# Performance work log

Measured on AMD Instinct MI355X. Metric: run time of the kernel, lower is better.

The kernel has to match this reference:

```python
import jax, jax.numpy as jnp
import numpy as np

D = 512      # d_model
H = 8        # num_heads
DH = D // H  # d_head = 64
WIN = 10     # window_size
DFF = 2048   # d_ff
EPS = 1e-5   # LayerNorm eps


def _layernorm(x, w, b):
    mu = jnp.mean(x, axis=-1, keepdims=True)
    var = jnp.mean(jnp.square(x - mu), axis=-1, keepdims=True)
    return (x - mu) * jax.lax.rsqrt(var + EPS) * w + b


def setup_inputs() -> dict:
    key = jax.random.key(0)
    ks = jax.random.split(key, 8)
    s = 0.02
    inp = {
        "z": jax.random.normal(ks[0], (4, 2048, D), jnp.float32),
        "Wq": jax.random.normal(ks[1], (D, D), jnp.float32) * s,
        "bq": jnp.zeros((D,), jnp.float32),
        "Wk": jax.random.normal(ks[2], (D, D), jnp.float32) * s,
        "bk": jnp.zeros((D,), jnp.float32),
        "Wv": jax.random.normal(ks[3], (D, D), jnp.float32) * s,
        "bv": jnp.zeros((D,), jnp.float32),
        "Wo": jax.random.normal(ks[4], (D, D), jnp.float32) * s,
        "bo": jnp.zeros((D,), jnp.float32),
        "ln1_w": jnp.ones((D,), jnp.float32),
        "ln1_b": jnp.zeros((D,), jnp.float32),
        "W1": jax.random.normal(ks[5], (D, DFF), jnp.float32) * s,
        "b1": jnp.zeros((DFF,), jnp.float32),
        "W2": jax.random.normal(ks[6], (DFF, D), jnp.float32) * s,
        "b2": jnp.zeros((D,), jnp.float32),
        "ln2_w": jnp.ones((D,), jnp.float32),
        "ln2_b": jnp.zeros((D,), jnp.float32),
    }
    return inp


def reference(z, Wq, bq, Wk, bk, Wv, bv, Wo, bo, ln1_w, ln1_b, W1, b1, W2, b2, ln2_w, ln2_b):
    B, T, Dm = z.shape
    # projections -> [B, H, T, DH]
    q = (z @ Wq + bq).reshape(B, T, H, DH).transpose(0, 2, 1, 3)
    k = (z @ Wk + bk).reshape(B, T, H, DH).transpose(0, 2, 1, 3)
    v = (z @ Wv + bv).reshape(B, T, H, DH).transpose(0, 2, 1, 3)
    scale = 1.0 / jnp.sqrt(jnp.asarray(DH, z.dtype))
    scores = jnp.einsum('bhqd,bhkd->bhqk', q, k) * scale  # [B,H,T,T]
    idx = jnp.arange(T)
    dist = idx[:, None] - idx[None, :]
    valid = (dist >= 0) & (dist < WIN)
    neg = jnp.finfo(scores.dtype).min
    scores = jnp.where(valid[None, None], scores, neg)
    attn = jax.nn.softmax(scores, axis=-1)  # dropout is identity in eval
    out = jnp.einsum('bhqk,bhkd->bhqd', attn, v)
    out = out.transpose(0, 2, 1, 3).reshape(B, T, Dm)
    out = out @ Wo + bo
    z = _layernorm(z + out, ln1_w, ln1_b)
    # FFN with exact (erf) GELU, matching torch nn.GELU default
    ff = jax.nn.gelu(z @ W1 + b1, approximate=False) @ W2 + b2
    z = _layernorm(z + ff, ln2_w, ln2_b)
    return z
```

## Files before the change

### kernel.cpp

```cpp
#include <hip/hip_runtime.h>
#include <cstdint>
#include <cstddef>

#define DEV __device__ __forceinline__

typedef __bf16 bf16x8 __attribute__((ext_vector_type(8)));
typedef float f32x4 __attribute__((ext_vector_type(4)));
typedef unsigned short us8 __attribute__((ext_vector_type(8)));
typedef unsigned short us4 __attribute__((ext_vector_type(4)));

typedef const __attribute__((address_space(1))) unsigned int GUI;
typedef __attribute__((address_space(3))) unsigned int LUI;

DEV unsigned short f2bf(float f) {
  unsigned int u = __builtin_bit_cast(unsigned int, f);
  u += 0x7fffu + ((u >> 16) & 1u);
  return (unsigned short)(u >> 16);
}
DEV float bf2f(unsigned short h) {
  unsigned int u = ((unsigned int)h) << 16;
  return __builtin_bit_cast(float, u);
}

DEV float gelu_exact(float x) {
  float xs = x * 0.70710678118654752f;
  float a = fabsf(xs);
  float t = __builtin_amdgcn_rcpf(fmaf(0.3275911f, a, 1.0f));
  float poly = t * fmaf(t, fmaf(t, fmaf(t, fmaf(t, 1.061405429f, -1.453152027f),
                                        1.421413741f), -0.284496736f), 0.254829592f);
  float erfa = 1.0f - poly * __expf(-a * a);
  float er = (xs < 0.f) ? -erfa : erfa;
  return 0.5f * x * (1.0f + er);
}

DEV void tr32(const float* __restrict__ in, unsigned short* __restrict__ out,
              int K, int N, int k0, int n0) {
  __shared__ float tile[32][33];
  const int tx = threadIdx.x & 31, ty = threadIdx.x >> 5;
#pragma unroll
  for (int i = 0; i < 32; i += 8)
    tile[ty + i][tx] = in[(size_t)(k0 + ty + i) * N + n0 + tx];
  __syncthreads();
#pragma unroll
  for (int i = 0; i < 32; i += 8)
    out[(size_t)(n0 + ty + i) * K + k0 + tx] = f2bf(tile[tx][ty + i]);
}

__global__ __launch_bounds__(256) void k_prep(
    const float* __restrict__ z, unsigned short* __restrict__ zb,
    const float* __restrict__ Wq, const float* __restrict__ Wk,
    const float* __restrict__ Wv, const float* __restrict__ Wo,
    unsigned short* __restrict__ Wsq,
    const float* __restrict__ W1, unsigned short* __restrict__ W1T,
    const float* __restrict__ W2, unsigned short* __restrict__ W2T,
    const float* __restrict__ bq, const float* __restrict__ bk,
    const float* __restrict__ bv, float* __restrict__ biasqkv) {
  const int j = blockIdx.x;
  const int tid = threadIdx.x;
  if (j < 4096) {
    int i = j * 256 + tid;
    float4 v = ((const float4*)z)[i];
    us4 o;
    o.x = f2bf(v.x); o.y = f2bf(v.y); o.z = f2bf(v.z); o.w = f2bf(v.w);
    *(us4*)(zb + (size_t)i * 4) = o;
  } else if (j < 5120) {
    int t = j - 4096;
    int mat = t >> 8, tile = t & 255;
    const float* in = mat == 0 ? Wq : mat == 1 ? Wk : mat == 2 ? Wv : Wo;
    tr32(in, Wsq + (size_t)mat * 262144, 512, 512, (tile >> 4) * 32, (tile & 15) * 32);
  } else if (j < 6144) {
    int t = j - 5120;
    tr32(W1, W1T, 512, 2048, (t / 64) * 32, (t % 64) * 32);
  } else if (j < 7168) {
    int t = j - 6144;
    tr32(W2, W2T, 2048, 512, (t / 16) * 32, (t % 16) * 32);
  } else {
    for (int i = tid; i < 1536; i += 256)
      biasqkv[i] = (i < 512) ? bq[i] : (i < 1024 ? bk[i - 512] : bv[i - 1024]);
  }
}

template <int MODE, int SPLITK>
DEV void gemm256_body(const unsigned short* __restrict__ A,
                      const unsigned short* __restrict__ BT,
                      const float* __restrict__ bias,
                      unsigned short* __restrict__ outp,
                      int K, int N) {
  __shared__ __align__(16) unsigned short As[2 * 16384];
  __shared__ __align__(16) unsigned short Bs[2 * 16384];
  const int tid = threadIdx.x;
  const int wave = tid >> 6, lane = tid & 63;
  const int wm = wave >> 2, wn = wave & 3;

  const int nx = gridDim.x, ny = gridDim.y;
  const int nwg = nx * ny * SPLITK;
  const int lid = (blockIdx.z * ny + blockIdx.y) * nx + blockIdx.x;
  const int q8 = nwg >> 3, r8 = nwg & 7;
  const int xcd = lid & 7, slot = lid >> 3;
  const int wid = (xcd < r8 ? xcd * (q8 + 1) : r8 * (q8 + 1) + (xcd - r8) * q8) + slot;
  const int nbz = nx * SPLITK;
  const int bxz = wid % nbz;
  const int by  = wid / nbz;
  const int bx  = bxz % nx;
  const int z   = bxz / nx;

  const int rbase = by * 256;
  const int nbase = bx * 256;
  const int nkt = (K / SPLITK) >> 6;
  const int kb = z * (K / SPLITK);

  float bv_[4];
#pragma unroll
  for (int n = 0; n < 4; ++n) {
    int gcol = nbase + wn * 64 + n * 16 + (lane & 15);
    bv_[n] = (z == 0) ? bias[gcol] : 0.f;
  }
  asm volatile("s_waitcnt vmcnt(0)" ::: "memory");

  auto STAGE = [&](int buf, int k0) {
#pragma unroll
    for (int t = 0; t < 4; ++t) {
      int s = t * 512 + tid;
      int row = s >> 3;
      int col = ((s & 7) ^ (row & 7)) << 3;
      const unsigned short* ga = A + (size_t)(rbase + row) * K + k0 + col;
      const unsigned short* gb = BT + (size_t)(nbase + row) * K + k0 + col;
      const int dst = buf * 16384 + (t * 512 + wave * 64) * 8;
      __builtin_amdgcn_global_load_lds((GUI*)ga, (LUI*)(As + dst), 16, 0, 0);
      __builtin_amdgcn_global_load_lds((GUI*)gb, (LUI*)(Bs + dst), 16, 0, 0);
    }
  };

  f32x4 acc[8][4] = {};
  STAGE(0, kb);

  for (int kt = 0; kt < nkt; ++kt) {
    const int cur = kt & 1;
    if (kt + 1 < nkt) {
      STAGE(cur ^ 1, kb + (kt + 1) * 64);
      asm volatile("s_waitcnt vmcnt(8)" ::: "memory");
    } else {
      asm volatile("s_waitcnt vmcnt(0)" ::: "memory");
    }
    __builtin_amdgcn_s_barrier();

#pragma unroll
    for (int ks = 0; ks < 2; ++ks) {
      bf16x8 af[8], bfr[4];
#pragma unroll
      for (int m = 0; m < 8; ++m) {
        int row = wm * 128 + m * 16 + (lane & 15);
        int ch = (ks * 4 + (lane >> 4)) ^ (row & 7);
        af[m] = __builtin_bit_cast(bf16x8, *(const us8*)(As + cur * 16384 + row * 64 + ch * 8));
      }
#pragma unroll
      for (int n = 0; n < 4; ++n) {
        int row = wn * 64 + n * 16 + (lane & 15);
        int ch = (ks * 4 + (lane >> 4)) ^ (row & 7);
        bfr[n] = __builtin_bit_cast(bf16x8, *(const us8*)(Bs + cur * 16384 + row * 64 + ch * 8));
      }
      __builtin_amdgcn_s_setprio(1);
#pragma unroll
      for (int m = 0; m < 8; ++m)
#pragma unroll
        for (int n = 0; n < 4; ++n)
          acc[m][n] = __builtin_amdgcn_mfma_f32_16x16x32_bf16(af[m], bfr[n], acc[m][n], 0, 0, 0);
      __builtin_amdgcn_s_setprio(0);
    }
    asm volatile("s_waitcnt lgkmcnt(0)" ::: "memory");
    __builtin_amdgcn_s_barrier();
  }

  unsigned short* opv = outp + (size_t)z * 8192 * N;
#pragma unroll
  for (int m = 0; m < 8; ++m) {
    int grow0 = rbase + wm * 128 + m * 16 + ((lane >> 4) << 2);
#pragma unroll
    for (int n = 0; n < 4; ++n) {
      int gcol = nbase + wn * 64 + n * 16 + (lane & 15);
#pragma unroll
      for (int r = 0; r < 4; ++r) {
        float v = acc[m][n][r] + bv_[n];
        if (MODE == 2) v = gelu_exact(v);
        opv[(size_t)(grow0 + r) * N + gcol] = f2bf(v);
      }
    }
  }
}

__global__ __launch_bounds__(512) void k_qkv(const unsigned short* __restrict__ A,
                                             const unsigned short* __restrict__ BT,
                                             const float* __restrict__ bias,
                                             unsigned short* __restrict__ outp, int K, int N) {
  gemm256_body<0, 1>(A, BT, bias, outp, K, N);
}
__global__ __launch_bounds__(512) void k_ffn1(const unsigned short* __restrict__ A,
                                              const unsigned short* __restrict__ BT,
                                              const float* __restrict__ bias,
                                              unsigned short* __restrict__ outp, int K, int N) {
  gemm256_body<2, 1>(A, BT, bias, outp, K, N);
}
__global__ __launch_bounds__(512) void k_ffn2(const unsigned short* __restrict__ A,
                                              const unsigned short* __restrict__ BT,
                                              const float* __restrict__ bias,
                                              unsigned short* __restrict__ outp, int K, int N) {
  gemm256_body<0, 4>(A, BT, bias, outp, K, N);
}

__global__ __launch_bounds__(512) void k_awl(
    const unsigned short* __restrict__ qkv,
    const unsigned short* __restrict__ WoT,
    const float* __restrict__ bo,
    const unsigned short* __restrict__ zb,
    const float* __restrict__ ln1w, const float* __restrict__ ln1b,
    unsigned short* __restrict__ z1b) {
  __shared__ __align__(16) char smem[137728];
  unsigned short* aout = (unsigned short*)smem;
  float* Kt = (float*)(smem + 33280);
  float* P  = (float*)(smem + 125440);
  unsigned short* Bst = (unsigned short*)(smem + 33280);
  float* part = (float*)(smem + 98816);
  float* lnp  = (float*)(smem + 100864);

  const int tid = threadIdx.x;
  const int w = tid >> 6, lane = tid & 63;
  const int bid = blockIdx.x;
  const int b = bid >> 6;
  const int i0 = (bid & 63) * 32;
  const int b2048 = b * 2048;
  const int h64 = w * 64;

  float* KtH = Kt + w * (64 * 45);
#pragma unroll 8
  for (int r = 0; r < 41; ++r) {
    int jloc = i0 - 9 + r;
    int jc = jloc < 0 ? 0 : jloc;
    KtH[lane * 45 + r] = bf2f(qkv[(size_t)(b2048 + jc) * 1536 + 512 + h64 + lane]);
  }
  const int qe = lane & 31, dh = lane >> 5;
  us8 qreg[4];
  {
    const unsigned short* qp = qkv + (size_t)(b2048 + i0 + qe) * 1536 + h64 + dh * 32;
#pragma unroll
    for (int t = 0; t < 4; ++t) qreg[t] = *(const us8*)(qp + t * 8);
  }
  float s[10];
#pragma unroll
  for (int jj = 0; jj < 10; ++jj) s[jj] = 0.f;
#pragma unroll
  for (int t = 0; t < 4; ++t) {
#pragma unroll
    for (int e = 0; e < 8; ++e) {
      float qd = bf2f(qreg[t][e]);
      int d = dh * 32 + t * 8 + e;
#pragma unroll
      for (int jj = 0; jj < 10; ++jj)
        s[jj] = fmaf(qd, KtH[d * 45 + qe + jj], s[jj]);
    }
  }
#pragma unroll
  for (int jj = 0; jj < 10; ++jj) s[jj] += __shfl_xor(s[jj], 32);
  const int iG = i0 + qe;
#pragma unroll
  for (int jj = 0; jj < 10; ++jj)
    s[jj] = (iG - 9 + jj >= 0) ? s[jj] * 0.125f : -1e30f;
  float mx = s[9];
#pragma unroll
  for (int jj = 0; jj < 9; ++jj) mx = fmaxf(mx, s[jj]);
  float den = 0.f;
#pragma unroll
  for (int jj = 0; jj < 10; ++jj) {
    s[jj] = __expf(s[jj] - mx);
    den += s[jj];
  }
  float inv = 1.f / den;
  if (lane < 32) {
#pragma unroll
    for (int jj = 0; jj < 10; ++jj) P[(w * 32 + qe) * 12 + jj] = s[jj] * inv;
  }
  for (int q0 = 0; q0 < 32; q0 += 4) {
    float vv[13];
#pragma unroll
    for (int t = 0; t < 13; ++t) {
      int jloc = i0 + q0 - 9 + t;
      int jc = jloc < 0 ? 0 : jloc;
      vv[t] = bf2f(qkv[(size_t)(b2048 + jc) * 1536 + 1024 + h64 + lane]);
    }
#pragma unroll
    for (int qq = 0; qq < 4; ++qq) {
      const int qy = q0 + qq;
      const float* pp = &P[(w * 32 + qy) * 12];
      float o = 0.f;
#pragma unroll
      for (int jj = 0; jj < 10; ++jj) o = fmaf(pp[jj], vv[qq + jj], o);
      aout[qy * 520 + h64 + lane] = f2bf(o);
    }
  }
  __syncthreads();

  const int q4 = lane >> 4, l15 = lane & 15;
  auto STAGE = [&](int buf, int k0) {
#pragma unroll
    for (int t = 0; t < 4; ++t) {
      int sI = t * 512 + tid;
      int R = sI >> 3;
      int c = (sI & 7) ^ (R & 7);
      int rr = 2 * R + (c >> 2);
      int kl = (c & 3) << 3;
      const unsigned short* gb = WoT + (size_t)rr * 512 + k0 + kl;
      const int dst = buf * 16384 + (t * 512 + w * 64) * 8;
      __builtin_amdgcn_global_load_lds((GUI*)gb, (LUI*)(Bst + dst), 16, 0, 0);
    }
  };
  asm volatile("s_waitcnt vmcnt(0)" ::: "memory");
  STAGE(0, 0);
  f32x4 acc[2][4] = {};
  for (int kt = 0; kt < 16; ++kt) {
    const int cur = kt & 1;
    if (kt + 1 < 16) {
      STAGE(cur ^ 1, (kt + 1) * 32);
      asm volatile("s_waitcnt vmcnt(4)" ::: "memory");
    } else {
      asm volatile("s_waitcnt vmcnt(0)" ::: "memory");
    }
    __builtin_amdgcn_s_barrier();
    bf16x8 af[2], bfr[4];
#pragma unroll
    for (int m = 0; m < 2; ++m) {
      int row = m * 16 + l15;
      af[m] = __builtin_bit_cast(bf16x8, *(const us8*)(aout + row * 520 + kt * 32 + q4 * 8));
    }
#pragma unroll
    for (int n = 0; n < 4; ++n) {
      int rr = h64 + n * 16 + l15;
      int R = rr >> 1;
      int d = (((rr & 1) << 2) + q4) ^ (R & 7);
      bfr[n] = __builtin_bit_cast(bf16x8, *(const us8*)(Bst + cur * 16384 + R * 64 + d * 8));
    }
    asm volatile("s_waitcnt lgkmcnt(0)" ::: "memory");
    __builtin_amdgcn_sched_barrier(0);
    __builtin_amdgcn_s_setprio(1);
#pragma unroll
    for (int m = 0; m < 2; ++m)
#pragma unroll
      for (int n = 0; n < 4; ++n)
        acc[m][n] = __builtin_amdgcn_mfma_f32_16x16x32_bf16(af[m], bfr[n], acc[m][n], 0, 0, 0);
    __builtin_amdgcn_s_setprio(0);
    __builtin_amdgcn_s_barrier();
  }

  float x[2][4][4];
  float psum[8], pss[8];
#pragma unroll
  for (int m = 0; m < 8; ++m) { psum[m] = 0.f; pss[m] = 0.f; }
#pragma unroll
  for (int m = 0; m < 2; ++m) {
#pragma unroll
    for (int n = 0; n < 4; ++n) {
      int col = h64 + n * 16 + l15;
      float bv = bo[col];
#pragma unroll
      for (int r = 0; r < 4; ++r) {
        int row = m * 16 + (q4 << 2) + r;
        float v = acc[m][n][r] + bv + bf2f(zb[(size_t)(b2048 + i0 + row) * 512 + col]);
        x[m][n][r] = v;
        psum[m * 4 + r] += v;
        pss[m * 4 + r] += v * v;
      }
    }
  }
#pragma unroll
  for (int m = 0; m < 8; ++m) {
#pragma unroll
    for (int o = 1; o < 16; o <<= 1) {
      psum[m] += __shfl_xor(psum[m], o);
      pss[m]  += __shfl_xor(pss[m], o);
    }
  }
  if (l15 == 0) {
#pragma unroll
    for (int m = 0; m < 2; ++m)
#pragma unroll
      for (int r = 0; r < 4; ++r) {
        int row = m * 16 + (q4 << 2) + r;
        part[(row * 8 + w) * 2 + 0] = psum[m * 4 + r];
        part[(row * 8 + w) * 2 + 1] = pss[m * 4 + r];
      }
  }
  __syncthreads();
  if (w == 0 && lane < 32) {
    float su = 0.f, ssq = 0.f;
#pragma unroll
    for (int p = 0; p < 8; ++p) {
      su  += part[(lane * 8 + p) * 2 + 0];
      ssq += part[(lane * 8 + p) * 2 + 1];
    }
    float mu = su * (1.f / 512.f);
    float var = ssq * (1.f / 512.f) - mu * mu;
    lnp[lane * 2 + 0] = mu;
    lnp[lane * 2 + 1] = rsqrtf(var + 1e-5f);
  }
  __syncthreads();
#pragma unroll
  for (int m = 0; m < 2; ++m) {
#pragma unroll
    for (int n = 0; n < 4; ++n) {
      int col = h64 + n * 16 + l15;
      float wv = ln1w[col], bbv = ln1b[col];
#pragma unroll
      for (int r = 0; r < 4; ++r) {
        int row = m * 16 + (q4 << 2) + r;
        float o = (x[m][n][r] - lnp[row * 2]) * lnp[row * 2 + 1] * wv + bbv;
        z1b[(size_t)(b2048 + i0 + row) * 512 + col] = f2bf(o);
      }
    }
  }
}

__global__ __launch_bounds__(256) void k_ln_out(const unsigned short* __restrict__ res,
                                                const unsigned short* __restrict__ add,
                                                const float* __restrict__ w,
                                                const float* __restrict__ bb,
                                                float* __restrict__ outp) {
  const size_t PLANE = (size_t)8192 * 512;
  const int wave = threadIdx.x >> 6, lane = threadIdx.x & 63;
  const int row = blockIdx.x * 4 + wave;
  float x[8];
  us8 r = *(const us8*)(res + (size_t)row * 512 + lane * 8);
#pragma unroll
  for (int j = 0; j < 8; ++j) x[j] = bf2f(r[j]);
#pragma unroll
  for (int p = 0; p < 4; ++p) {
    us8 a = *(const us8*)(add + p * PLANE + (size_t)row * 512 + lane * 8);
#pragma unroll
    for (int j = 0; j < 8; ++j) x[j] += bf2f(a[j]);
  }
  float sum = 0.f, ss = 0.f;
#pragma unroll
  for (int j = 0; j < 8; ++j) {
    sum += x[j];
    ss += x[j] * x[j];
  }
#pragma unroll
  for (int m = 32; m >= 1; m >>= 1) {
    sum += __shfl_xor(sum, m);
    ss += __shfl_xor(ss, m);
  }
  const float mu = sum * (1.f / 512.f);
  float var = ss * (1.f / 512.f) - mu * mu;
  const float rstd = rsqrtf(var + 1e-5f);
  const int c = lane * 8;
  float4 u0, u1;
  float o[8];
#pragma unroll
  for (int j = 0; j < 8; ++j) o[j] = (x[j] - mu) * rstd * w[c + j] + bb[c + j];
  u0.x = o[0]; u0.y = o[1]; u0.z = o[2]; u0.w = o[3];
  u1.x = o[4]; u1.y = o[5]; u1.z = o[6]; u1.w = o[7];
  float4* o4 = (float4*)(outp + (size_t)row * 512 + c);
  o4[0] = u0; o4[1] = u1;
}

extern "C" void kernel_launch(void* const* d_in, const int* in_sizes, int n_in,
                              void* d_out, int out_size, void* d_ws, size_t ws_size,
                              hipStream_t stream) {
  const float* z    = (const float*)d_in[0];
  const float* Wq   = (const float*)d_in[1];
  const float* bq   = (const float*)d_in[2];
  const float* Wk   = (const float*)d_in[3];
  const float* bk   = (const float*)d_in[4];
  const float* Wv   = (const float*)d_in[5];
  const float* bv   = (const float*)d_in[6];
  const float* Wo   = (const float*)d_in[7];
  const float* bo   = (const float*)d_in[8];
  const float* ln1w = (const float*)d_in[9];
  const float* ln1b = (const float*)d_in[10];
  const float* W1   = (const float*)d_in[11];
  const float* b1   = (const float*)d_in[12];
  const float* W2   = (const float*)d_in[13];
  const float* b2   = (const float*)d_in[14];
  const float* ln2w = (const float*)d_in[15];
  const float* ln2b = (const float*)d_in[16];
  float* out = (float*)d_out;

  char* ws = (char*)d_ws;
  size_t off = 0;
  auto alloc = [&](size_t bytes) {
    char* p = ws + off;
    off += (bytes + 255) & ~(size_t)255;
    return p;
  };
  unsigned short* Wsq   = (unsigned short*)alloc((size_t)2048 * 512 * 2);
  unsigned short* WTqkv = Wsq;
  unsigned short* WoT   = Wsq + (size_t)1536 * 512;
  unsigned short* W1T   = (unsigned short*)alloc((size_t)2048 * 512 * 2);
  unsigned short* W2T   = (unsigned short*)alloc((size_t)512 * 2048 * 2);
  float*          biasqkv = (float*)alloc(1536 * 4);
  unsigned short* zb    = (unsigned short*)alloc((size_t)8192 * 512 * 2);
  unsigned short* z1b   = (unsigned short*)alloc((size_t)8192 * 512 * 2);
  unsigned short* qkvb  = (unsigned short*)alloc((size_t)8192 * 1536 * 2);
  unsigned short* p1    = (unsigned short*)alloc((size_t)4 * 8192 * 512 * 2);
  unsigned short* ff    = qkvb;

  k_prep<<<7169, 256, 0, stream>>>(z, zb, Wq, Wk, Wv, Wo, Wsq, W1, W1T, W2, W2T,
                                   bq, bk, bv, biasqkv);
  k_qkv<<<dim3(6, 32), 512, 0, stream>>>(zb, WTqkv, biasqkv, qkvb, 512, 1536);
  k_awl<<<256, 512, 0, stream>>>(qkvb, WoT, bo, zb, ln1w, ln1b, z1b);
  k_ffn1<<<dim3(8, 32), 512, 0, stream>>>(z1b, W1T, b1, ff, 512, 2048);
  k_ffn2<<<dim3(2, 32, 4), 512, 0, stream>>>(ff, W2T, b2, p1, 2048, 512);
  k_ln_out<<<2048, 256, 0, stream>>>(z1b, p1, ln2w, ln2b, out);
}
```

Measured before the change: 125.1 us.

## Fuse FFN2 GEMM with residual add and LayerNorm, drop split-K partials

```diff
diff --git a/kernel.cpp b/kernel.cpp
--- a/kernel.cpp
+++ b/kernel.cpp
@@ -80,7 +80,7 @@
   }
 }
 
-template <int MODE, int SPLITK>
+template <int MODE>
 DEV void gemm256_body(const unsigned short* __restrict__ A,
                       const unsigned short* __restrict__ BT,
                       const float* __restrict__ bias,
@@ -93,28 +93,22 @@
   const int wm = wave >> 2, wn = wave & 3;
 
   const int nx = gridDim.x, ny = gridDim.y;
-  const int nwg = nx * ny * SPLITK;
-  const int lid = (blockIdx.z * ny + blockIdx.y) * nx + blockIdx.x;
+  const int nwg = nx * ny;
+  const int lid = blockIdx.y * nx + blockIdx.x;
   const int q8 = nwg >> 3, r8 = nwg & 7;
   const int xcd = lid & 7, slot = lid >> 3;
   const int wid = (xcd < r8 ? xcd * (q8 + 1) : r8 * (q8 + 1) + (xcd - r8) * q8) + slot;
-  const int nbz = nx * SPLITK;
-  const int bxz = wid % nbz;
-  const int by  = wid / nbz;
-  const int bx  = bxz % nx;
-  const int z   = bxz / nx;
+  const int bx  = wid % nx;
+  const int by  = wid / nx;
 
   const int rbase = by * 256;
   const int nbase = bx * 256;
-  const int nkt = (K / SPLITK) >> 6;
-  const int kb = z * (K / SPLITK);
+  const int nkt = K >> 6;
 
   float bv_[4];
 #pragma unroll
-  for (int n = 0; n < 4; ++n) {
-    int gcol = nbase + wn * 64 + n * 16 + (lane & 15);
-    bv_[n] = (z == 0) ? bias[gcol] : 0.f;
-  }
+  for (int n = 0; n < 4; ++n)
+    bv_[n] = bias[nbase + wn * 64 + n * 16 + (lane & 15)];
   asm volatile("s_waitcnt vmcnt(0)" ::: "memory");
 
   auto STAGE = [&](int buf, int k0) {
@@ -132,12 +126,12 @@
   };
 
   f32x4 acc[8][4] = {};
-  STAGE(0, kb);
+  STAGE(0, 0);
 
   for (int kt = 0; kt < nkt; ++kt) {
     const int cur = kt & 1;
     if (kt + 1 < nkt) {
-      STAGE(cur ^ 1, kb + (kt + 1) * 64);
+      STAGE(cur ^ 1, (kt + 1) * 64);
       asm volatile("s_waitcnt vmcnt(8)" ::: "memory");
     } else {
       asm volatile("s_waitcnt vmcnt(0)" ::: "memory");
@@ -171,7 +165,6 @@
     __builtin_amdgcn_s_barrier();
   }
 
-  unsigned short* opv = outp + (size_t)z * 8192 * N;
 #pragma unroll
   for (int m = 0; m < 8; ++m) {
     int grow0 = rbase + wm * 128 + m * 16 + ((lane >> 4) << 2);
@@ -182,7 +175,7 @@
       for (int r = 0; r < 4; ++r) {
         float v = acc[m][n][r] + bv_[n];
         if (MODE == 2) v = gelu_exact(v);
-        opv[(size_t)(grow0 + r) * N + gcol] = f2bf(v);
+        outp[(size_t)(grow0 + r) * N + gcol] = f2bf(v);
       }
     }
   }
@@ -192,19 +185,13 @@
                                              const unsigned short* __restrict__ BT,
                                              const float* __restrict__ bias,
                                              unsigned short* __restrict__ outp, int K, int N) {
-  gemm256_body<0, 1>(A, BT, bias, outp, K, N);
+  gemm256_body<0>(A, BT, bias, outp, K, N);
 }
 __global__ __launch_bounds__(512) void k_ffn1(const unsigned short* __restrict__ A,
                                               const unsigned short* __restrict__ BT,
                                               const float* __restrict__ bias,
                                               unsigned short* __restrict__ outp, int K, int N) {
-  gemm256_body<2, 1>(A, BT, bias, outp, K, N);
-}
-__global__ __launch_bounds__(512) void k_ffn2(const unsigned short* __restrict__ A,
-                                              const unsigned short* __restrict__ BT,
-                                              const float* __restrict__ bias,
-                                              unsigned short* __restrict__ outp, int K, int N) {
-  gemm256_body<0, 4>(A, BT, bias, outp, K, N);
+  gemm256_body<2>(A, BT, bias, outp, K, N);
 }
 
 __global__ __launch_bounds__(512) void k_awl(
@@ -417,47 +404,159 @@
   }
 }
 
-__global__ __launch_bounds__(256) void k_ln_out(const unsigned short* __restrict__ res,
-                                                const unsigned short* __restrict__ add,
-                                                const float* __restrict__ w,
-                                                const float* __restrict__ bb,
-                                                float* __restrict__ outp) {
-  const size_t PLANE = (size_t)8192 * 512;
-  const int wave = threadIdx.x >> 6, lane = threadIdx.x & 63;
-  const int row = blockIdx.x * 4 + wave;
-  float x[8];
-  us8 r = *(const us8*)(res + (size_t)row * 512 + lane * 8);
-#pragma unroll
-  for (int j = 0; j < 8; ++j) x[j] = bf2f(r[j]);
-#pragma unroll
-  for (int p = 0; p < 4; ++p) {
-    us8 a = *(const us8*)(add + p * PLANE + (size_t)row * 512 + lane * 8);
-#pragma unroll
-    for (int j = 0; j < 8; ++j) x[j] += bf2f(a[j]);
-  }
-  float sum = 0.f, ss = 0.f;
-#pragma unroll
-  for (int j = 0; j < 8; ++j) {
-    sum += x[j];
-    ss += x[j] * x[j];
-  }
-#pragma unroll
-  for (int m = 32; m >= 1; m >>= 1) {
-    sum += __shfl_xor(sum, m);
-    ss += __shfl_xor(ss, m);
-  }
-  const float mu = sum * (1.f / 512.f);
-  float var = ss * (1.f / 512.f) - mu * mu;
-  const float rstd = rsqrtf(var + 1e-5f);
-  const int c = lane * 8;
-  float4 u0, u1;
-  float o[8];
-#pragma unroll
-  for (int j = 0; j < 8; ++j) o[j] = (x[j] - mu) * rstd * w[c + j] + bb[c + j];
-  u0.x = o[0]; u0.y = o[1]; u0.z = o[2]; u0.w = o[3];
-  u1.x = o[4]; u1.y = o[5]; u1.z = o[6]; u1.w = o[7];
-  float4* o4 = (float4*)(outp + (size_t)row * 512 + c);
-  o4[0] = u0; o4[1] = u1;
+__global__ __launch_bounds__(512) void k_f2l(
+    const unsigned short* __restrict__ ff,
+    const unsigned short* __restrict__ W2T,
+    const float* __restrict__ b2,
+    const unsigned short* __restrict__ z1b,
+    const float* __restrict__ ln2w, const float* __restrict__ ln2b,
+    float* __restrict__ outp) {
+  __shared__ __align__(16) unsigned short Bst[2 * 16384];
+  __shared__ __align__(16) unsigned short Ast[2 * 1024];
+  __shared__ float part[32 * 8 * 2];
+  __shared__ float lnp[32 * 2];
+
+  const int tid = threadIdx.x;
+  const int w = tid >> 6, lane = tid & 63;
+  const int bid = blockIdx.x;
+  const int b = bid >> 6;
+  const int i0 = (bid & 63) * 32;
+  const int b2048 = b * 2048;
+  const int q4 = lane >> 4, l15 = lane & 15;
+  const int w64 = w * 64;
+
+  auto STAGE = [&](int buf, int k0) {
+#pragma unroll
+    for (int t = 0; t < 4; ++t) {
+      int sI = t * 512 + tid;
+      int R = sI >> 3;
+      int c = (sI & 7) ^ (R & 7);
+      int rr = 2 * R + (c >> 2);
+      int kl = (c & 3) << 3;
+      const unsigned short* gb = W2T + (size_t)rr * 2048 + k0 + kl;
+      const int dst = buf * 16384 + (t * 512 + w64) * 8;
+      __builtin_amdgcn_global_load_lds((GUI*)gb, (LUI*)(Bst + dst), 16, 0, 0);
+    }
+    if (w < 2) {
+      int sI = tid;
+      int R = sI >> 3;
+      int c = (sI & 7) ^ (R & 7);
+      int rr = 2 * R + (c >> 2);
+      int kl = (c & 3) << 3;
+      const unsigned short* ga = ff + (size_t)(b2048 + i0 + rr) * 2048 + k0 + kl;
+      const int dst = buf * 1024 + w64 * 8;
+      __builtin_amdgcn_global_load_lds((GUI*)ga, (LUI*)(Ast + dst), 16, 0, 0);
+    }
+  };
+
+  asm volatile("s_waitcnt vmcnt(0)" ::: "memory");
+  STAGE(0, 0);
+  f32x4 acc[2][4] = {};
+
+  for (int kt = 0; kt < 64; ++kt) {
+    const int cur = kt & 1;
+    if (kt + 1 < 64) {
+      STAGE(cur ^ 1, (kt + 1) * 32);
+      if (w < 2) asm volatile("s_waitcnt vmcnt(5)" ::: "memory");
+      else       asm volatile("s_waitcnt vmcnt(4)" ::: "memory");
+    } else {
+      asm volatile("s_waitcnt vmcnt(0)" ::: "memory");
+    }
+    __builtin_amdgcn_s_barrier();
+
+    bf16x8 af[2], bfr[4];
+#pragma unroll
+    for (int m = 0; m < 2; ++m) {
+      int rowr = m * 16 + l15;
+      int R = rowr >> 1;
+      int d = (((rowr & 1) << 2) + q4) ^ (R & 7);
+      af[m] = __builtin_bit_cast(bf16x8, *(const us8*)(Ast + cur * 1024 + R * 64 + d * 8));
+    }
+#pragma unroll
+    for (int n = 0; n < 4; ++n) {
+      int rr = w64 + n * 16 + l15;
+      int R = rr >> 1;
+      int d = (((rr & 1) << 2) + q4) ^ (R & 7);
+      bfr[n] = __builtin_bit_cast(bf16x8, *(const us8*)(Bst + cur * 16384 + R * 64 + d * 8));
+    }
+    asm volatile("s_waitcnt lgkmcnt(0)" ::: "memory");
+    __builtin_amdgcn_sched_barrier(0);
+    __builtin_amdgcn_s_setprio(1);
+#pragma unroll
+    for (int m = 0; m < 2; ++m)
+#pragma unroll
+      for (int n = 0; n < 4; ++n)
+        acc[m][n] = __builtin_amdgcn_mfma_f32_16x16x32_bf16(af[m], bfr[n], acc[m][n], 0, 0, 0);
+    __builtin_amdgcn_s_setprio(0);
+    __builtin_amdgcn_s_barrier();
+  }
+
+  float x[2][4][4];
+  float psum[8], pss[8];
+#pragma unroll
+  for (int m = 0; m < 8; ++m) { psum[m] = 0.f; pss[m] = 0.f; }
+#pragma unroll
+  for (int m = 0; m < 2; ++m) {
+#pragma unroll
+    for (int n = 0; n < 4; ++n) {
+      int col = w64 + n * 16 + l15;
+      float bv = b2[col];
+#pragma unroll
+      for (int r = 0; r < 4; ++r) {
+        int row = m * 16 + (q4 << 2) + r;
+        float v = acc[m][n][r] + bv + bf2f(z1b[(size_t)(b2048 + i0 + row) * 512 + col]);
+        x[m][n][r] = v;
+        psum[m * 4 + r] += v;
+        pss[m * 4 + r] += v * v;
+      }
+    }
+  }
+#pragma unroll
+  for (int m = 0; m < 8; ++m) {
+#pragma unroll
+    for (int o = 1; o < 16; o <<= 1) {
+      psum[m] += __shfl_xor(psum[m], o);
+      pss[m]  += __shfl_xor(pss[m], o);
+    }
+  }
+  if (l15 == 0) {
+#pragma unroll
+    for (int m = 0; m < 2; ++m)
+#pragma unroll
+      for (int r = 0; r < 4; ++r) {
+        int row = m * 16 + (q4 << 2) + r;
+        part[(row * 8 + w) * 2 + 0] = psum[m * 4 + r];
+        part[(row * 8 + w) * 2 + 1] = pss[m * 4 + r];
+      }
+  }
+  __syncthreads();
+  if (w == 0 && lane < 32) {
+    float su = 0.f, ssq = 0.f;
+#pragma unroll
+    for (int p = 0; p < 8; ++p) {
+      su  += part[(lane * 8 + p) * 2 + 0];
+      ssq += part[(lane * 8 + p) * 2 + 1];
+    }
+    float mu = su * (1.f / 512.f);
+    float var = ssq * (1.f / 512.f) - mu * mu;
+    lnp[lane * 2 + 0] = mu;
+    lnp[lane * 2 + 1] = rsqrtf(var + 1e-5f);
+  }
+  __syncthreads();
+#pragma unroll
+  for (int m = 0; m < 2; ++m) {
+#pragma unroll
+    for (int n = 0; n < 4; ++n) {
+      int col = w64 + n * 16 + l15;
+      float wv = ln2w[col], bbv = ln2b[col];
+#pragma unroll
+      for (int r = 0; r < 4; ++r) {
+        int row = m * 16 + (q4 << 2) + r;
+        float o = (x[m][n][r] - lnp[row * 2]) * lnp[row * 2 + 1] * wv + bbv;
+        outp[(size_t)(b2048 + i0 + row) * 512 + col] = o;
+      }
+    }
+  }
 }
 
 extern "C" void kernel_launch(void* const* d_in, const int* in_sizes, int n_in,
@@ -498,7 +597,6 @@
   unsigned short* zb    = (unsigned short*)alloc((size_t)8192 * 512 * 2);
   unsigned short* z1b   = (unsigned short*)alloc((size_t)8192 * 512 * 2);
   unsigned short* qkvb  = (unsigned short*)alloc((size_t)8192 * 1536 * 2);
-  unsigned short* p1    = (unsigned short*)alloc((size_t)4 * 8192 * 512 * 2);
   unsigned short* ff    = qkvb;
 
   k_prep<<<7169, 256, 0, stream>>>(z, zb, Wq, Wk, Wv, Wo, Wsq, W1, W1T, W2, W2T,
@@ -506,6 +604,5 @@
   k_qkv<<<dim3(6, 32), 512, 0, stream>>>(zb, WTqkv, biasqkv, qkvb, 512, 1536);
   k_awl<<<256, 512, 0, stream>>>(qkvb, WoT, bo, zb, ln1w, ln1b, z1b);
   k_ffn1<<<dim3(8, 32), 512, 0, stream>>>(z1b, W1T, b1, ff, 512, 2048);
-  k_ffn2<<<dim3(2, 32, 4), 512, 0, stream>>>(ff, W2T, b2, p1, 2048, 512);
-  k_ln_out<<<2048, 256, 0, stream>>>(z1b, p1, ln2w, ln2b, out);
-}
+  k_f2l<<<256, 512, 0, stream>>>(ff, W2T, b2, z1b, ln2w, ln2b, out);
+}
```

Result: slower. 152.4 us (+21.8%).

## Replace split-K FFN2 GEMM with 128x128 tile kernel and single output

Applied to the files above, without the earlier changes.

```diff
diff --git a/kernel.cpp b/kernel.cpp
--- a/kernel.cpp
+++ b/kernel.cpp
@@ -80,7 +80,7 @@
   }
 }
 
-template <int MODE, int SPLITK>
+template <int MODE>
 DEV void gemm256_body(const unsigned short* __restrict__ A,
                       const unsigned short* __restrict__ BT,
                       const float* __restrict__ bias,
@@ -93,28 +93,22 @@
   const int wm = wave >> 2, wn = wave & 3;
 
   const int nx = gridDim.x, ny = gridDim.y;
-  const int nwg = nx * ny * SPLITK;
-  const int lid = (blockIdx.z * ny + blockIdx.y) * nx + blockIdx.x;
+  const int nwg = nx * ny;
+  const int lid = blockIdx.y * nx + blockIdx.x;
   const int q8 = nwg >> 3, r8 = nwg & 7;
   const int xcd = lid & 7, slot = lid >> 3;
   const int wid = (xcd < r8 ? xcd * (q8 + 1) : r8 * (q8 + 1) + (xcd - r8) * q8) + slot;
-  const int nbz = nx * SPLITK;
-  const int bxz = wid % nbz;
-  const int by  = wid / nbz;
-  const int bx  = bxz % nx;
-  const int z   = bxz / nx;
+  const int bx  = wid % nx;
+  const int by  = wid / nx;
 
   const int rbase = by * 256;
   const int nbase = bx * 256;
-  const int nkt = (K / SPLITK) >> 6;
-  const int kb = z * (K / SPLITK);
+  const int nkt = K >> 6;
 
   float bv_[4];
 #pragma unroll
-  for (int n = 0; n < 4; ++n) {
-    int gcol = nbase + wn * 64 + n * 16 + (lane & 15);
-    bv_[n] = (z == 0) ? bias[gcol] : 0.f;
-  }
+  for (int n = 0; n < 4; ++n)
+    bv_[n] = bias[nbase + wn * 64 + n * 16 + (lane & 15)];
   asm volatile("s_waitcnt vmcnt(0)" ::: "memory");
 
   auto STAGE = [&](int buf, int k0) {
@@ -132,12 +126,12 @@
   };
 
   f32x4 acc[8][4] = {};
-  STAGE(0, kb);
+  STAGE(0, 0);
 
   for (int kt = 0; kt < nkt; ++kt) {
     const int cur = kt & 1;
     if (kt + 1 < nkt) {
-      STAGE(cur ^ 1, kb + (kt + 1) * 64);
+      STAGE(cur ^ 1, (kt + 1) * 64);
       asm volatile("s_waitcnt vmcnt(8)" ::: "memory");
     } else {
       asm volatile("s_waitcnt vmcnt(0)" ::: "memory");
@@ -171,7 +165,6 @@
     __builtin_amdgcn_s_barrier();
   }
 
-  unsigned short* opv = outp + (size_t)z * 8192 * N;
 #pragma unroll
   for (int m = 0; m < 8; ++m) {
     int grow0 = rbase + wm * 128 + m * 16 + ((lane >> 4) << 2);
@@ -182,7 +175,108 @@
       for (int r = 0; r < 4; ++r) {
         float v = acc[m][n][r] + bv_[n];
         if (MODE == 2) v = gelu_exact(v);
-        opv[(size_t)(grow0 + r) * N + gcol] = f2bf(v);
+        outp[(size_t)(grow0 + r) * N + gcol] = f2bf(v);
+      }
+    }
+  }
+}
+
+template <int MODE>
+DEV void gemm128_body(const unsigned short* __restrict__ A,
+                      const unsigned short* __restrict__ BT,
+                      const float* __restrict__ bias,
+                      unsigned short* __restrict__ outp,
+                      int K, int N) {
+  __shared__ __align__(16) unsigned short As[2 * 8192];
+  __shared__ __align__(16) unsigned short Bs[2 * 8192];
+  const int tid = threadIdx.x;
+  const int wave = tid >> 6, lane = tid & 63;
+  const int wm = wave >> 1, wn = wave & 1;
+  const int q = lane >> 4, l15 = lane & 15;
+
+  const int nx = gridDim.x, ny = gridDim.y;
+  const int nwg = nx * ny;
+  const int lid = blockIdx.y * nx + blockIdx.x;
+  const int q8 = nwg >> 3, r8 = nwg & 7;
+  const int xcd = lid & 7, slot = lid >> 3;
+  const int wid = (xcd < r8 ? xcd * (q8 + 1) : r8 * (q8 + 1) + (xcd - r8) * q8) + slot;
+  const int bx = wid % nx;
+  const int by = wid / nx;
+
+  const int rbase = by * 128;
+  const int nbase = bx * 128;
+  const int nkt = K >> 6;
+
+  float bv_[4];
+#pragma unroll
+  for (int n = 0; n < 4; ++n) bv_[n] = bias[nbase + wn * 64 + n * 16 + l15];
+  asm volatile("s_waitcnt vmcnt(0)" ::: "memory");
+
+  auto STAGE = [&](int buf, int k0) {
+#pragma unroll
+    for (int t = 0; t < 4; ++t) {
+      int s = t * 256 + tid;
+      int row = s >> 3;
+      int col = ((s & 7) ^ (row & 7)) << 3;
+      const unsigned short* ga = A + (size_t)(rbase + row) * K + k0 + col;
+      const unsigned short* gb = BT + (size_t)(nbase + row) * K + k0 + col;
+      const int dst = buf * 8192 + (t * 256 + wave * 64) * 8;
+      __builtin_amdgcn_global_load_lds((GUI*)ga, (LUI*)(As + dst), 16, 0, 0);
+      __builtin_amdgcn_global_load_lds((GUI*)gb, (LUI*)(Bs + dst), 16, 0, 0);
+    }
+  };
+
+  f32x4 acc[4][4] = {};
+  STAGE(0, 0);
+
+  for (int kt = 0; kt < nkt; ++kt) {
+    const int cur = kt & 1;
+    if (kt + 1 < nkt) {
+      STAGE(cur ^ 1, (kt + 1) * 64);
+      asm volatile("s_waitcnt vmcnt(8)" ::: "memory");
+    } else {
+      asm volatile("s_waitcnt vmcnt(0)" ::: "memory");
+    }
+    __builtin_amdgcn_s_barrier();
+
+#pragma unroll
+    for (int ks = 0; ks < 2; ++ks) {
+      bf16x8 af[4], bfr[4];
+#pragma unroll
+      for (int m = 0; m < 4; ++m) {
+        int row = wm * 64 + m * 16 + l15;
+        int ch = (ks * 4 + q) ^ (row & 7);
+        af[m] = __builtin_bit_cast(bf16x8, *(const us8*)(As + cur * 8192 + row * 64 + ch * 8));
+      }
+#pragma unroll
+      for (int n = 0; n < 4; ++n) {
+        int row = wn * 64 + n * 16 + l15;
+        int ch = (ks * 4 + q) ^ (row & 7);
+        bfr[n] = __builtin_bit_cast(bf16x8, *(const us8*)(Bs + cur * 8192 + row * 64 + ch * 8));
+      }
+      __builtin_amdgcn_s_setprio(1);
+#pragma unroll
+      for (int m = 0; m < 4; ++m)
+#pragma unroll
+        for (int n = 0; n < 4; ++n)
+          acc[m][n] = __builtin_amdgcn_mfma_f32_16x16x32_bf16(af[m], bfr[n], acc[m][n], 0, 0, 0);
+      __builtin_amdgcn_s_setprio(0);
+    }
+    asm volatile("s_waitcnt lgkmcnt(0)" ::: "memory");
+    __builtin_amdgcn_s_barrier();
+  }
+
+#pragma unroll
+  for (int m = 0; m < 4; ++m) {
+    int grow0 = rbase + wm * 64 + m * 16 + (q << 2);
+#pragma unroll
+    for (int n = 0; n < 4; ++n) {
+      int gcol = nbase + wn * 64 + n * 16 + l15;
+#pragma unroll
+      for (int r = 0; r < 4; ++r) {
+        float v = acc[m][n][r] + bv_[n];
+        if (MODE == 2) v = gelu_exact(v);
+        outp[(size_t)(grow0 + r) * N + gcol] = f2bf(v);
       }
     }
   }
@@ -192,19 +286,19 @@
                                              const unsigned short* __restrict__ BT,
                                              const float* __restrict__ bias,
                                              unsigned short* __restrict__ outp, int K, int N) {
-  gemm256_body<0, 1>(A, BT, bias, outp, K, N);
+  gemm256_body<0>(A, BT, bias, outp, K, N);
 }
 __global__ __launch_bounds__(512) void k_ffn1(const unsigned short* __restrict__ A,
                                               const unsigned short* __restrict__ BT,
                                               const float* __restrict__ bias,
                                               unsigned short* __restrict__ outp, int K, int N) {
-  gemm256_body<2, 1>(A, BT, bias, outp, K, N);
-}
-__global__ __launch_bounds__(512) void k_ffn2(const unsigned short* __restrict__ A,
+  gemm256_body<2>(A, BT, bias, outp, K, N);
+}
+__global__ __launch_bounds__(256) void k_ffn2(const unsigned short* __restrict__ A,
                                               const unsigned short* __restrict__ BT,
                                               const float* __restrict__ bias,
                                               unsigned short* __restrict__ outp, int K, int N) {
-  gemm256_body<0, 4>(A, BT, bias, outp, K, N);
+  gemm128_body<0>(A, BT, bias, outp, K, N);
 }
 
 __global__ __launch_bounds__(512) void k_awl(
@@ -422,22 +516,15 @@
                                                 const float* __restrict__ w,
                                                 const float* __restrict__ bb,
                                                 float* __restrict__ outp) {
-  const size_t PLANE = (size_t)8192 * 512;
   const int wave = threadIdx.x >> 6, lane = threadIdx.x & 63;
   const int row = blockIdx.x * 4 + wave;
   float x[8];
   us8 r = *(const us8*)(res + (size_t)row * 512 + lane * 8);
-#pragma unroll
-  for (int j = 0; j < 8; ++j) x[j] = bf2f(r[j]);
-#pragma unroll
-  for (int p = 0; p < 4; ++p) {
-    us8 a = *(const us8*)(add + p * PLANE + (size_t)row * 512 + lane * 8);
-#pragma unroll
-    for (int j = 0; j < 8; ++j) x[j] += bf2f(a[j]);
-  }
+  us8 a = *(const us8*)(add + (size_t)row * 512 + lane * 8);
   float sum = 0.f, ss = 0.f;
 #pragma unroll
   for (int j = 0; j < 8; ++j) {
+    x[j] = bf2f(r[j]) + bf2f(a[j]);
     sum += x[j];
     ss += x[j] * x[j];
   }
@@ -498,7 +585,7 @@
   unsigned short* zb    = (unsigned short*)alloc((size_t)8192 * 512 * 2);
   unsigned short* z1b   = (unsigned short*)alloc((size_t)8192 * 512 * 2);
   unsigned short* qkvb  = (unsigned short*)alloc((size_t)8192 * 1536 * 2);
-  unsigned short* p1    = (unsigned short*)alloc((size_t)4 * 8192 * 512 * 2);
+  unsigned short* f2out = (unsigned short*)alloc((size_t)8192 * 512 * 2);
   unsigned short* ff    = qkvb;
 
   k_prep<<<7169, 256, 0, stream>>>(z, zb, Wq, Wk, Wv, Wo, Wsq, W1, W1T, W2, W2T,
@@ -506,6 +593,6 @@
   k_qkv<<<dim3(6, 32), 512, 0, stream>>>(zb, WTqkv, biasqkv, qkvb, 512, 1536);
   k_awl<<<256, 512, 0, stream>>>(qkvb, WoT, bo, zb, ln1w, ln1b, z1b);
   k_ffn1<<<dim3(8, 32), 512, 0, stream>>>(z1b, W1T, b1, ff, 512, 2048);
-  k_ffn2<<<dim3(2, 32, 4), 512, 0, stream>>>(ff, W2T, b2, p1, 2048, 512);
-  k_ln_out<<<2048, 256, 0, stream>>>(z1b, p1, ln2w, ln2b, out);
-}
+  k_ffn2<<<dim3(4, 64), 256, 0, stream>>>(ff, W2T, b2, f2out, 2048, 512);
+  k_ln_out<<<2048, 256, 0, stream>>>(z1b, f2out, ln2w, ln2b, out);
+}
```

After: 133.5 us. 6.7% more time.
